# Kernel tuning notes

Hardware: AMD Instinct MI355X
Metric: run time of the kernel (lower is better)

Reference implementation:

```python
import math
import jax, jax.numpy as jnp
import numpy as np

EMBED_DIM = 768
NUM_HEADS = 12
HEAD_DIM = EMBED_DIM // NUM_HEADS


def setup_inputs() -> dict:
    key = jax.random.key(0)
    ks = jax.random.split(key, 9)
    R, C, B, E = 128, 512, 1, EMBED_DIM
    x = jax.random.normal(ks[0], (R, C, B, E), dtype=jnp.float32)
    s = 0.02
    # weights stored so that projection is x @ W + b (i.e. torch Linear weight transposed)
    Wq = jax.random.normal(ks[1], (E, E), dtype=jnp.float32) * s
    Wk = jax.random.normal(ks[2], (E, E), dtype=jnp.float32) * s
    Wv = jax.random.normal(ks[3], (E, E), dtype=jnp.float32) * s
    Wo = jax.random.normal(ks[4], (E, E), dtype=jnp.float32) * s
    bq = jnp.zeros((E,), jnp.float32)
    bk = jnp.zeros((E,), jnp.float32)
    bv = jnp.zeros((E,), jnp.float32)
    bo = jnp.zeros((E,), jnp.float32)
    return {"x": x, "Wq": Wq, "bq": bq, "Wk": Wk, "bk": bk,
            "Wv": Wv, "bv": bv, "Wo": Wo, "bo": bo}


def reference(x, Wq, bq, Wk, bk, Wv, bv, Wo, bo):
    R, C, B, E = x.shape
    H, D = NUM_HEADS, HEAD_DIM
    # scaling = head_dim^-0.5 / sqrt(num_rows)  (align_scaling)
    scaling = (D ** -0.5) / math.sqrt(R)
    q = (x @ Wq + bq).reshape(R, C, B, H, D) * scaling
    k = (x @ Wk + bk).reshape(R, C, B, H, D)
    v = (x @ Wv + bv).reshape(R, C, B, H, D)
    # sum attention logits over rows r -> shared [h, n, i, j] attention map
    attn_weights = jnp.einsum('rinhd,rjnhd->hnij', q, k)
    attn_probs = jax.nn.softmax(attn_weights, axis=-1)
    context = jnp.einsum('hnij,rjnhd->rinhd', attn_probs, v)
    context = context.reshape(R, C, B, E)
    output = context @ Wo + bo
    return output, attn_probs
```

## Files before the change

kernel.cpp:

```cpp
#include <hip/hip_runtime.h>
#include <math.h>

#define RDIM 128
#define CDIM 512
#define EDIM 768
#define HDIM 12
#define DDIM 64
#define MDIM (RDIM*CDIM)
#define OUT_ELEMS ((size_t)MDIM*EDIM)
#define HSTRIDE ((size_t)CDIM*RDIM*DDIM)
#define WELEMS (EDIM*EDIM)

typedef unsigned short ushort_t;
typedef __attribute__((ext_vector_type(8))) short bf16x8;
typedef __attribute__((ext_vector_type(8))) unsigned short u16x8;
typedef __attribute__((ext_vector_type(4))) float f32x4;

__device__ __forceinline__ ushort_t f2bf(float f) {
    unsigned u = __float_as_uint(f);
    unsigned r = u + 0x7fffu + ((u >> 16) & 1u);
    return (ushort_t)(r >> 16);
}

__device__ __forceinline__ void gload16(const void* g, void* l) {
    __builtin_amdgcn_global_load_lds(
        (const __attribute__((address_space(1))) unsigned int*)g,
        (__attribute__((address_space(3))) unsigned int*)l, 16, 0, 0);
}

__global__ __launch_bounds__(256)
void cast_x(const float* __restrict__ x, ushort_t* __restrict__ xb) {
    size_t i = ((size_t)blockIdx.x * 256 + threadIdx.x) * 8;
    float4 a = *(const float4*)&x[i];
    float4 b = *(const float4*)&x[i + 4];
    u16x8 o;
    o[0]=f2bf(a.x); o[1]=f2bf(a.y); o[2]=f2bf(a.z); o[3]=f2bf(a.w);
    o[4]=f2bf(b.x); o[5]=f2bf(b.y); o[6]=f2bf(b.z); o[7]=f2bf(b.w);
    *(u16x8*)&xb[i] = o;
}

__global__ __launch_bounds__(256)
void transpose_cast_w(const float* __restrict__ W, ushort_t* __restrict__ Wt) {
    __shared__ ushort_t t[64][66];
    const int k0 = blockIdx.x * 64, n0 = blockIdx.y * 64;
    const int tx = threadIdx.x & 15, ty = threadIdx.x >> 4;
    #pragma unroll
    for (int rep = 0; rep < 4; ++rep) {
        int k = ty + rep * 16;
        float4 v = *(const float4*)&W[(size_t)(k0 + k) * EDIM + n0 + tx*4];
        t[k][tx*4+0] = f2bf(v.x); t[k][tx*4+1] = f2bf(v.y);
        t[k][tx*4+2] = f2bf(v.z); t[k][tx*4+3] = f2bf(v.w);
    }
    __syncthreads();
    #pragma unroll
    for (int rep = 0; rep < 4; ++rep) {
        int n = ty + rep * 16;
        ushort4 o = { t[tx*4+0][n], t[tx*4+1][n], t[tx*4+2][n], t[tx*4+3][n] };
        *(ushort4*)&Wt[(size_t)(n0 + n) * EDIM + k0 + tx*4] = o;
    }
}

__global__ __launch_bounds__(256)
void concat_bias(const float* __restrict__ bq, const float* __restrict__ bk,
                 const float* __restrict__ bv, float* __restrict__ bqkv) {
    int i = blockIdx.x * 256 + threadIdx.x;
    if (i < 768)        bqkv[i] = bq[i];
    else if (i < 1536)  bqkv[i] = bk[i - 768];
    else if (i < 2304)  bqkv[i] = bv[i - 1536];
}

#define SBAR do { __builtin_amdgcn_sched_barrier(0); \
                  __builtin_amdgcn_s_barrier(); \
                  __builtin_amdgcn_sched_barrier(0); } while(0)
#define SCHED0 __builtin_amdgcn_sched_barrier(0)
#define VMCNT(n_) asm volatile("s_waitcnt vmcnt(" #n_ ")" ::: "memory")

template<int M, int N, int K, int LDK, int MODE, int NWG>
__global__ __launch_bounds__(512, 2)
void gemm8(const ushort_t* __restrict__ A, const ushort_t* __restrict__ B,
           const float* __restrict__ bias, float scale,
           float* __restrict__ outF, ushort_t* __restrict__ outB,
           size_t sAh, size_t sBh) {
    __shared__ __align__(16) char smem[131072];
    constexpr int NT = K / 64;

    const int tid = threadIdx.x;
    const int lane = tid & 63, wid = tid >> 6;
    const int wr = wid >> 2, wc = wid & 3;
    const int fr = lane & 15, fs = lane >> 4;
    const int sw = (fr & 7) << 3;

    const int bid = blockIdx.x;
    const int w = (bid & 7) * (NWG / 8) + (bid >> 3);
    int bm, bn, h = 0, ksub = 0, plane = 0, ntile = 0;
    if (MODE == 4)      { ntile = w % 9; bm = (w / 9) * 256; bn = ntile * 256; }
    else if (MODE == 2) { plane = w >> 2; h = plane >> 3; ksub = plane & 7;
                          bm = ((w >> 1) & 1) * 256; bn = (w & 1) * 256; }
    else if (MODE == 3) { h = w >> 6; bm = ((w >> 5) & 1) * 256; bn = (w & 31) * 256; }
    else                { bm = (w / 3) * 256; bn = (w % 3) * 256; }

    const ushort_t* Ab = A + (MODE == 2 || MODE == 3 ? (size_t)h * sAh : 0)
                       + (MODE == 2 ? (size_t)ksub * K : 0) + (size_t)bm * LDK;
    const ushort_t* Bb = B + (MODE == 2 || MODE == 3 ? (size_t)h * sBh : 0)
                       + (MODE == 2 ? (size_t)ksub * K : 0) + (size_t)bn * LDK;

    const int r0 = tid >> 3, s0 = tid & 7;
    const size_t gO0 = (size_t)r0 * LDK + ((s0 ^ (r0 & 7)) * 8);
    const size_t gO1 = gO0 + (size_t)64 * LDK;
    const int l0 = tid * 16, l1 = tid * 16 + 8192;

#define STAGE_A(t_, h_) do { \
    char* d_ = smem + ((((t_) & 1) * 2 + (h_)) * 16384); \
    const ushort_t* s_ = Ab + (size_t)((h_) * 128) * LDK + (t_) * 64; \
    gload16(s_ + gO0, d_ + l0); gload16(s_ + gO1, d_ + l1); } while(0)
#define STAGE_B(t_, h_) do { \
    char* d_ = smem + 65536 + ((((t_) & 1) * 2 + (h_)) * 16384); \
    const ushort_t* s_ = Bb + (size_t)((h_) * 128) * LDK + (t_) * 64; \
    gload16(s_ + gO0, d_ + l0); gload16(s_ + gO1, d_ + l1); } while(0)

    f32x4 acc[8][4];
    #pragma unroll
    for (int i = 0; i < 8; ++i)
        #pragma unroll
        for (int j = 0; j < 4; ++j) acc[i][j] = (f32x4){0.f, 0.f, 0.f, 0.f};
    bf16x8 a_[4][2], bb0_[2][2], bb1_[2][2];

#define DSA(t_, mq_) do { \
    const ushort_t* As_ = (const ushort_t*)(smem + ((((t_) & 1) * 2 + wr) * 16384)); \
    _Pragma("unroll") for (int f = 0; f < 4; ++f) \
      _Pragma("unroll") for (int kk = 0; kk < 2; ++kk) \
        a_[f][kk] = *(const bf16x8*)&As_[((mq_) * 64 + f * 16 + fr) * 64 \
                                          + ((kk * 32 + fs * 8) ^ sw)]; } while(0)

#define DSB(t_, nq_, B_) do { \
    const ushort_t* Bs_ = (const ushort_t*)(smem + 65536 + ((((t_) & 1) * 2 + (wc >> 1)) * 16384)); \
    _Pragma("unroll") for (int nf = 0; nf < 2; ++nf) \
      _Pragma("unroll") for (int kk = 0; kk < 2; ++kk) \
        B_[nf][kk] = *(const bf16x8*)&Bs_[((wc & 1) * 64 + (nq_) * 32 + nf * 16 + fr) * 64 \
                                           + ((kk * 32 + fs * 8) ^ sw)]; } while(0)

#define MFMA8(mq_, nq_, B_) do { \
    __builtin_amdgcn_s_setprio(1); \
    _Pragma("unroll") for (int f = 0; f < 4; ++f) \
      _Pragma("unroll") for (int nf2 = 0; nf2 < 2; ++nf2) \
        _Pragma("unroll") for (int kk = 0; kk < 2; ++kk) \
          acc[(mq_) * 4 + f][(nq_) * 2 + nf2] = __builtin_amdgcn_mfma_f32_16x16x32_bf16( \
              a_[f][kk], B_[nf2][kk], acc[(mq_) * 4 + f][(nq_) * 2 + nf2], 0, 0, 0); \
    __builtin_amdgcn_s_setprio(0); } while(0)

    STAGE_B(0, 0); SCHED0;
    STAGE_B(0, 1); SCHED0;
    STAGE_A(0, 0); SCHED0;
    STAGE_A(0, 1); SCHED0;
    STAGE_B(1, 0); SCHED0;
    STAGE_B(1, 1); SCHED0;
    STAGE_A(1, 0); SCHED0;
    STAGE_A(1, 1); SCHED0;
    VMCNT(8);
    SBAR;

    for (int t = 0; t < NT - 2; ++t) {
        DSA(t, 0); DSB(t, 0, bb0_);
        MFMA8(0, 0, bb0_);
        SBAR;
        DSB(t, 1, bb1_);
        MFMA8(0, 1, bb1_);
        SBAR;
        DSA(t, 1);
        STAGE_B(t + 2, 0); STAGE_B(t + 2, 1);
        MFMA8(1, 0, bb0_);
        SBAR;
        STAGE_A(t + 2, 0); STAGE_A(t + 2, 1);
        MFMA8(1, 1, bb1_);
        VMCNT(8);
        SBAR;
    }

    {
        const int t = NT - 2;
        DSA(t, 0); DSB(t, 0, bb0_); MFMA8(0, 0, bb0_); SBAR;
        DSB(t, 1, bb1_);            MFMA8(0, 1, bb1_); SBAR;
        DSA(t, 1);                  MFMA8(1, 0, bb0_); SBAR;
        MFMA8(1, 1, bb1_);
        VMCNT(0);
        SBAR;
        const int u = NT - 1;
        DSA(u, 0); DSB(u, 0, bb0_); MFMA8(0, 0, bb0_); SBAR;
        DSB(u, 1, bb1_);            MFMA8(0, 1, bb1_); SBAR;
        DSA(u, 1);                  MFMA8(1, 0, bb0_); SBAR;
        MFMA8(1, 1, bb1_);
    }

    if (MODE == 4) {
        const int which = ntile / 3;
        const int hcb = (ntile % 3) * 256;
        if (which < 2) {
            ushort_t* dst = outB + (size_t)which * OUT_ELEMS;
            const float sc = (which == 0) ? scale : 1.f;
            #pragma unroll
            for (int mf = 0; mf < 8; ++mf) {
                #pragma unroll
                for (int nf = 0; nf < 4; ++nf) {
                    const int hcol = hcb + wc*64 + nf*16 + fr;
                    const float bv = bias[which*768 + hcol];
                    const int hh = hcol >> 6, d = hcol & 63;
                    #pragma unroll
                    for (int j = 0; j < 4; ++j) {
                        const int m = bm + wr*128 + mf*16 + fs*4 + j;
                        float v = (acc[mf][nf][j] + bv) * sc;
                        size_t addr = (size_t)hh * HSTRIDE
                                    + (size_t)(m & 511) * 8192 + (m >> 9) * 64 + d;
                        dst[addr] = f2bf(v);
                    }
                }
            }
        } else {
            ushort_t* Ts = (ushort_t*)smem;
            ushort_t* dst = outB + 2 * OUT_ELEMS;
            const int rblk = bm >> 9, jb = bm & 511;
            __syncthreads();
            #pragma unroll
            for (int q = 0; q < 2; ++q) {
                if ((wc >> 1) == q) {
                    #pragma unroll
                    for (int mf = 0; mf < 8; ++mf) {
                        #pragma unroll
                        for (int nf = 0; nf < 4; ++nf) {
                            const int nl = wc*64 + nf*16 + fr;
                            const float bv = bias[1536 + hcb + nl];
                            #pragma unroll
                            for (int j = 0; j < 4; ++j)
                                Ts[(nl & 127)*264 + wr*128 + mf*16 + fs*4 + j] =
                                    f2bf(acc[mf][nf][j] + bv);
                        }
                    }
                }
                __syncthreads();
                #pragma unroll
                for (int it = 0; it < 8; ++it) {
                    const int idx = it * 512 + tid;
                    const int row = idx >> 5, c8 = (idx & 31) * 8;
                    const int nl = q*128 + row;
                    const int hh = (hcb + nl) >> 6, d = nl & 63;
                    uint4 wv;
                    wv.x = *(const uint*)&Ts[row*264 + c8];
                    wv.y = *(const uint*)&Ts[row*264 + c8 + 2];
                    wv.z = *(const uint*)&Ts[row*264 + c8 + 4];
                    wv.w = *(const uint*)&Ts[row*264 + c8 + 6];
                    size_t addr = (size_t)hh * HSTRIDE
                                + (size_t)(rblk*64 + d) * CDIM + jb + c8;
                    *(uint4*)&dst[addr] = wv;
                }
                __syncthreads();
            }
        }
        return;
    }

    #pragma unroll
    for (int mf = 0; mf < 8; ++mf) {
        #pragma unroll
        for (int nf = 0; nf < 4; ++nf) {
            const int n = bn + wc*64 + nf*16 + fr;
            float bv = (MODE == 1) ? bias[n] : 0.f;
            #pragma unroll
            for (int j = 0; j < 4; ++j) {
                const int m = bm + wr*128 + mf*16 + fs*4 + j;
                float v = acc[mf][nf][j];
                if (MODE == 1) {
                    outF[(size_t)m * N + n] = v + bv;
                } else if (MODE == 2) {
                    outF[(size_t)plane * (CDIM*CDIM) + (size_t)m * CDIM + n] = v;
                } else {
                    size_t addr = ((size_t)(n >> 6) * CDIM + m) * EDIM
                                + h * DDIM + (n & 63);
                    outB[addr] = f2bf(v);
                }
            }
        }
    }
}

__global__ __launch_bounds__(256)
void softmax_reduce(const float* __restrict__ part, float* __restrict__ attn,
                    ushort_t* __restrict__ Pb) {
    const int row = blockIdx.x;
    const int h = row >> 9, c = row & 511;
    const int tid = threadIdx.x;
    const int lane = tid & 63, wid = tid >> 6;
    __shared__ float red[8];

    float v0 = 0.f, v1 = 0.f;
    #pragma unroll
    for (int s = 0; s < 8; ++s) {
        const float* p = part + ((size_t)(h*8 + s) * (CDIM*CDIM)) + (size_t)c * CDIM;
        v0 += p[tid];
        v1 += p[tid + 256];
    }
    float m = fmaxf(v0, v1);
    #pragma unroll
    for (int off = 32; off > 0; off >>= 1) m = fmaxf(m, __shfl_down(m, off));
    if (lane == 0) red[wid] = m;
    __syncthreads();
    if (tid == 0) red[4] = fmaxf(fmaxf(red[0], red[1]), fmaxf(red[2], red[3]));
    __syncthreads();
    const float M = red[4];

    float e0 = expf(v0 - M), e1 = expf(v1 - M);
    float s = e0 + e1;
    #pragma unroll
    for (int off = 32; off > 0; off >>= 1) s += __shfl_down(s, off);
    __syncthreads();
    if (lane == 0) red[wid] = s;
    __syncthreads();
    if (tid == 0) red[5] = red[0] + red[1] + red[2] + red[3];
    __syncthreads();
    const float inv = 1.f / red[5];
    float o0 = e0 * inv, o1 = e1 * inv;
    float* pout = attn + (size_t)row * CDIM;
    ushort_t* pb = Pb + (size_t)row * CDIM;
    pout[tid] = o0;        pout[tid + 256] = o1;
    pb[tid]   = f2bf(o0);  pb[tid + 256]   = f2bf(o1);
}

extern "C" void kernel_launch(void* const* d_in, const int* in_sizes, int n_in,
                              void* d_out, int out_size, void* d_ws, size_t ws_size,
                              hipStream_t stream) {
    const float* x  = (const float*)d_in[0];
    const float* Wq = (const float*)d_in[1];
    const float* bq = (const float*)d_in[2];
    const float* Wk = (const float*)d_in[3];
    const float* bk = (const float*)d_in[4];
    const float* Wv = (const float*)d_in[5];
    const float* bv = (const float*)d_in[6];
    const float* Wo = (const float*)d_in[7];
    const float* bo = (const float*)d_in[8];

    float* out   = (float*)d_out;
    float* attnp = out + OUT_ELEMS;

    ushort_t* ws   = (ushort_t*)d_ws;
    ushort_t* xb   = ws;
    ushort_t* Wqkv = xb + OUT_ELEMS;
    ushort_t* Wto  = Wqkv + 3*WELEMS;
    float*    bqkv = (float*)(Wto + WELEMS);
    ushort_t* Qp   = Wto + WELEMS + 4608;
    ushort_t* Kp   = Qp + OUT_ELEMS;
    ushort_t* Vt   = Kp + OUT_ELEMS;
    ushort_t* Pb   = Vt + OUT_ELEMS;
    float*    part = (float*)xb;
    ushort_t* ctxb = xb;

    const float scaling = 0.011048543456039806f;

    cast_x<<<MDIM*EDIM/(256*8), 256, 0, stream>>>(x, xb);
    dim3 wt(EDIM/64, EDIM/64);
    transpose_cast_w<<<wt, 256, 0, stream>>>(Wq, Wqkv);
    transpose_cast_w<<<wt, 256, 0, stream>>>(Wk, Wqkv + WELEMS);
    transpose_cast_w<<<wt, 256, 0, stream>>>(Wv, Wqkv + 2*WELEMS);
    transpose_cast_w<<<wt, 256, 0, stream>>>(Wo, Wto);
    concat_bias<<<9, 256, 0, stream>>>(bq, bk, bv, bqkv);

    gemm8<MDIM, 2304, EDIM, EDIM, 4, 2304><<<2304, 512, 0, stream>>>(
        xb, Wqkv, bqkv, scaling, nullptr, Qp, 0, 0);

    gemm8<CDIM, CDIM, 1024, 8192, 2, 384><<<384, 512, 0, stream>>>(
        Qp, Kp, nullptr, 1.f, part, nullptr, HSTRIDE, HSTRIDE);

    softmax_reduce<<<HDIM*CDIM, 256, 0, stream>>>(part, attnp, Pb);

    gemm8<CDIM, 8192, CDIM, CDIM, 3, 768><<<768, 512, 0, stream>>>(
        Pb, Vt, nullptr, 1.f, nullptr, ctxb, (size_t)CDIM*CDIM, HSTRIDE);

    gemm8<MDIM, EDIM, EDIM, EDIM, 1, 768><<<768, 512, 0, stream>>>(
        ctxb, Wto, bo, 1.f, out, nullptr, 0, 0);
}
```

Baseline: 581.8 us.

## Software-pipeline LDS fragment loads one stage ahead of MFMA in GEMM main loop

Adds a second A-fragment register set and reorders the main loop so each LDS read (the B fragments for the next quarter, the A fragments for the next half, and the first A/B fragments of the next k-tile) is issued one MFMA block ahead of its use. The aim is to hide LDS read latency behind MFMA work instead of stalling right before each MFMA group. The global-load wait moves earlier and becomes a full vmcnt(0), and register pressure rises from the extra fragment buffers, which may lower occupancy.

```diff
diff --git a/kernel.cpp b/kernel.cpp
--- a/kernel.cpp
+++ b/kernel.cpp
@@ -123,13 +123,13 @@
     for (int i = 0; i < 8; ++i)
         #pragma unroll
         for (int j = 0; j < 4; ++j) acc[i][j] = (f32x4){0.f, 0.f, 0.f, 0.f};
-    bf16x8 a_[4][2], bb0_[2][2], bb1_[2][2];
-
-#define DSA(t_, mq_) do { \
+    bf16x8 a_[4][2], a2_[4][2], bb0_[2][2], bb1_[2][2];
+
+#define DSA(t_, mq_, A_) do { \
     const ushort_t* As_ = (const ushort_t*)(smem + ((((t_) & 1) * 2 + wr) * 16384)); \
     _Pragma("unroll") for (int f = 0; f < 4; ++f) \
       _Pragma("unroll") for (int kk = 0; kk < 2; ++kk) \
-        a_[f][kk] = *(const bf16x8*)&As_[((mq_) * 64 + f * 16 + fr) * 64 \
+        A_[f][kk] = *(const bf16x8*)&As_[((mq_) * 64 + f * 16 + fr) * 64 \
                                           + ((kk * 32 + fs * 8) ^ sw)]; } while(0)
 
 #define DSB(t_, nq_, B_) do { \
@@ -139,13 +139,13 @@
         B_[nf][kk] = *(const bf16x8*)&Bs_[((wc & 1) * 64 + (nq_) * 32 + nf * 16 + fr) * 64 \
                                            + ((kk * 32 + fs * 8) ^ sw)]; } while(0)
 
-#define MFMA8(mq_, nq_, B_) do { \
+#define MFMA8(mq_, nq_, A_, B_) do { \
     __builtin_amdgcn_s_setprio(1); \
     _Pragma("unroll") for (int f = 0; f < 4; ++f) \
       _Pragma("unroll") for (int nf2 = 0; nf2 < 2; ++nf2) \
         _Pragma("unroll") for (int kk = 0; kk < 2; ++kk) \
           acc[(mq_) * 4 + f][(nq_) * 2 + nf2] = __builtin_amdgcn_mfma_f32_16x16x32_bf16( \
-              a_[f][kk], B_[nf2][kk], acc[(mq_) * 4 + f][(nq_) * 2 + nf2], 0, 0, 0); \
+              A_[f][kk], B_[nf2][kk], acc[(mq_) * 4 + f][(nq_) * 2 + nf2], 0, 0, 0); \
     __builtin_amdgcn_s_setprio(0); } while(0)
 
     STAGE_B(0, 0); SCHED0;
@@ -158,37 +158,38 @@
     STAGE_A(1, 1); SCHED0;
     VMCNT(8);
     SBAR;
+    DSA(0, 0, a_); DSB(0, 0, bb0_);
 
     for (int t = 0; t < NT - 2; ++t) {
-        DSA(t, 0); DSB(t, 0, bb0_);
-        MFMA8(0, 0, bb0_);
+        DSB(t, 1, bb1_);
+        MFMA8(0, 0, a_, bb0_);
         SBAR;
-        DSB(t, 1, bb1_);
-        MFMA8(0, 1, bb1_);
+        DSA(t, 1, a2_);
+        MFMA8(0, 1, a_, bb1_);
+        VMCNT(0);
         SBAR;
-        DSA(t, 1);
+        DSA(t + 1, 0, a_);
         STAGE_B(t + 2, 0); STAGE_B(t + 2, 1);
-        MFMA8(1, 0, bb0_);
+        MFMA8(1, 0, a2_, bb0_);
         SBAR;
+        DSB(t + 1, 0, bb0_);
         STAGE_A(t + 2, 0); STAGE_A(t + 2, 1);
-        MFMA8(1, 1, bb1_);
-        VMCNT(8);
+        MFMA8(1, 1, a2_, bb1_);
         SBAR;
     }
 
     {
         const int t = NT - 2;
-        DSA(t, 0); DSB(t, 0, bb0_); MFMA8(0, 0, bb0_); SBAR;
-        DSB(t, 1, bb1_);            MFMA8(0, 1, bb1_); SBAR;
-        DSA(t, 1);                  MFMA8(1, 0, bb0_); SBAR;
-        MFMA8(1, 1, bb1_);
-        VMCNT(0);
-        SBAR;
+        DSB(t, 1, bb1_);      MFMA8(0, 0, a_, bb0_);  SBAR;
+        DSA(t, 1, a2_);       MFMA8(0, 1, a_, bb1_);
+        VMCNT(0);             SBAR;
+        DSA(t + 1, 0, a_);    MFMA8(1, 0, a2_, bb0_); SBAR;
+        DSB(t + 1, 0, bb0_);  MFMA8(1, 1, a2_, bb1_); SBAR;
         const int u = NT - 1;
-        DSA(u, 0); DSB(u, 0, bb0_); MFMA8(0, 0, bb0_); SBAR;
-        DSB(u, 1, bb1_);            MFMA8(0, 1, bb1_); SBAR;
-        DSA(u, 1);                  MFMA8(1, 0, bb0_); SBAR;
-        MFMA8(1, 1, bb1_);
+        DSB(u, 1, bb1_);      MFMA8(0, 0, a_, bb0_);  SBAR;
+        DSA(u, 1, a2_);       MFMA8(0, 1, a_, bb1_);  SBAR;
+        MFMA8(1, 0, a2_, bb0_);
+        MFMA8(1, 1, a2_, bb1_);
     }
 
     if (MODE == 4) {
```

New measurement: 598.0 us. 1.03x slower.

## Switch GEMMs to 256x128 tiles with B fragments loaded directly from global

Applied to the files above, without the earlier changes.

Replaces the 512-thread 256x256-tile GEMM with a 256-thread 256x128-tile variant. Only A is staged through LDS, with a two-buffer schedule. B fragments now go straight from global memory into registers, double-buffered across k-steps, which removes the B LDS traffic and cuts shared memory use. The risk is uncoalesced, unswizzled global reads for B that can stall the MFMA pipeline. The V-transpose epilogue is also simplified to a single pass.

```diff
diff --git a/kernel.cpp b/kernel.cpp
--- a/kernel.cpp
+++ b/kernel.cpp
@@ -76,54 +76,55 @@
 #define VMCNT(n_) asm volatile("s_waitcnt vmcnt(" #n_ ")" ::: "memory")
 
 template<int M, int N, int K, int LDK, int MODE, int NWG>
-__global__ __launch_bounds__(512, 2)
-void gemm8(const ushort_t* __restrict__ A, const ushort_t* __restrict__ B,
+__global__ __launch_bounds__(256, 2)
+void gemm2(const ushort_t* __restrict__ A, const ushort_t* __restrict__ B,
            const float* __restrict__ bias, float scale,
            float* __restrict__ outF, ushort_t* __restrict__ outB,
            size_t sAh, size_t sBh) {
-    __shared__ __align__(16) char smem[131072];
+    __shared__ __align__(16) char smem[69632];
     constexpr int NT = K / 64;
 
     const int tid = threadIdx.x;
     const int lane = tid & 63, wid = tid >> 6;
-    const int wr = wid >> 2, wc = wid & 3;
+    const int wr = wid >> 1, wc = wid & 1;
     const int fr = lane & 15, fs = lane >> 4;
     const int sw = (fr & 7) << 3;
 
     const int bid = blockIdx.x;
     const int w = (bid & 7) * (NWG / 8) + (bid >> 3);
     int bm, bn, h = 0, ksub = 0, plane = 0, ntile = 0;
-    if (MODE == 4)      { ntile = w % 9; bm = (w / 9) * 256; bn = ntile * 256; }
-    else if (MODE == 2) { plane = w >> 2; h = plane >> 3; ksub = plane & 7;
-                          bm = ((w >> 1) & 1) * 256; bn = (w & 1) * 256; }
-    else if (MODE == 3) { h = w >> 6; bm = ((w >> 5) & 1) * 256; bn = (w & 31) * 256; }
-    else                { bm = (w / 3) * 256; bn = (w % 3) * 256; }
+    if (MODE == 4)      { ntile = w % 18; bm = (w / 18) * 256; bn = ntile * 128; }
+    else if (MODE == 2) { plane = w >> 3; h = plane >> 3; ksub = plane & 7;
+                          bm = ((w >> 2) & 1) * 256; bn = (w & 3) * 128; }
+    else if (MODE == 3) { h = w >> 7; bm = ((w >> 6) & 1) * 256; bn = (w & 63) * 128; }
+    else                { bm = (w / 6) * 256; bn = (w % 6) * 128; }
 
     const ushort_t* Ab = A + (MODE == 2 || MODE == 3 ? (size_t)h * sAh : 0)
                        + (MODE == 2 ? (size_t)ksub * K : 0) + (size_t)bm * LDK;
     const ushort_t* Bb = B + (MODE == 2 || MODE == 3 ? (size_t)h * sBh : 0)
                        + (MODE == 2 ? (size_t)ksub * K : 0) + (size_t)bn * LDK;
 
-    const int r0 = tid >> 3, s0 = tid & 7;
-    const size_t gO0 = (size_t)r0 * LDK + ((s0 ^ (r0 & 7)) * 8);
-    const size_t gO1 = gO0 + (size_t)64 * LDK;
-    const int l0 = tid * 16, l1 = tid * 16 + 8192;
+    size_t gOf[4]; int lOf[4];
+    #pragma unroll
+    for (int j = 0; j < 4; ++j) {
+        int ci = j * 256 + tid;
+        int row = ci >> 3, seg = ci & 7;
+        gOf[j] = (size_t)row * LDK + (size_t)(((seg ^ (row & 7)) * 8));
+        lOf[j] = ci * 16;
+    }
 
 #define STAGE_A(t_, h_) do { \
     char* d_ = smem + ((((t_) & 1) * 2 + (h_)) * 16384); \
     const ushort_t* s_ = Ab + (size_t)((h_) * 128) * LDK + (t_) * 64; \
-    gload16(s_ + gO0, d_ + l0); gload16(s_ + gO1, d_ + l1); } while(0)
-#define STAGE_B(t_, h_) do { \
-    char* d_ = smem + 65536 + ((((t_) & 1) * 2 + (h_)) * 16384); \
-    const ushort_t* s_ = Bb + (size_t)((h_) * 128) * LDK + (t_) * 64; \
-    gload16(s_ + gO0, d_ + l0); gload16(s_ + gO1, d_ + l1); } while(0)
+    gload16(s_ + gOf[0], d_ + lOf[0]); gload16(s_ + gOf[1], d_ + lOf[1]); \
+    gload16(s_ + gOf[2], d_ + lOf[2]); gload16(s_ + gOf[3], d_ + lOf[3]); } while(0)
 
     f32x4 acc[8][4];
     #pragma unroll
     for (int i = 0; i < 8; ++i)
         #pragma unroll
         for (int j = 0; j < 4; ++j) acc[i][j] = (f32x4){0.f, 0.f, 0.f, 0.f};
-    bf16x8 a_[4][2], bb0_[2][2], bb1_[2][2];
+    bf16x8 a_[4][2], bb0x[2][2], bb1x[2][2], bb0y[2][2], bb1y[2][2];
 
 #define DSA(t_, mq_) do { \
     const ushort_t* As_ = (const ushort_t*)(smem + ((((t_) & 1) * 2 + wr) * 16384)); \
@@ -132,12 +133,11 @@
         a_[f][kk] = *(const bf16x8*)&As_[((mq_) * 64 + f * 16 + fr) * 64 \
                                           + ((kk * 32 + fs * 8) ^ sw)]; } while(0)
 
-#define DSB(t_, nq_, B_) do { \
-    const ushort_t* Bs_ = (const ushort_t*)(smem + 65536 + ((((t_) & 1) * 2 + (wc >> 1)) * 16384)); \
+#define BLOAD(t_, nq_, B_) do { \
     _Pragma("unroll") for (int nf = 0; nf < 2; ++nf) \
       _Pragma("unroll") for (int kk = 0; kk < 2; ++kk) \
-        B_[nf][kk] = *(const bf16x8*)&Bs_[((wc & 1) * 64 + (nq_) * 32 + nf * 16 + fr) * 64 \
-                                           + ((kk * 32 + fs * 8) ^ sw)]; } while(0)
+        B_[nf][kk] = *(const bf16x8*)(Bb + (size_t)(wc*64 + (nq_)*32 + nf*16 + fr) * LDK \
+                                         + (t_)*64 + kk*32 + fs*8); } while(0)
 
 #define MFMA8(mq_, nq_, B_) do { \
     __builtin_amdgcn_s_setprio(1); \
@@ -148,52 +148,37 @@
               a_[f][kk], B_[nf2][kk], acc[(mq_) * 4 + f][(nq_) * 2 + nf2], 0, 0, 0); \
     __builtin_amdgcn_s_setprio(0); } while(0)
 
-    STAGE_B(0, 0); SCHED0;
-    STAGE_B(0, 1); SCHED0;
-    STAGE_A(0, 0); SCHED0;
-    STAGE_A(0, 1); SCHED0;
-    STAGE_B(1, 0); SCHED0;
-    STAGE_B(1, 1); SCHED0;
-    STAGE_A(1, 0); SCHED0;
-    STAGE_A(1, 1); SCHED0;
+#define TILE(t_, C0_, C1_, N0_, N1_, STG_, BLD_, VM_) do { \
+    DSA(t_, 0); \
+    if (STG_) { STAGE_A((t_) + 1, 0); STAGE_A((t_) + 1, 1); } \
+    MFMA8(0, 0, C0_); \
+    MFMA8(0, 1, C1_); \
+    SBAR; \
+    DSA(t_, 1); \
+    if (BLD_) { BLOAD((t_) + 1, 0, N0_); BLOAD((t_) + 1, 1, N1_); } \
+    MFMA8(1, 0, C0_); \
+    MFMA8(1, 1, C1_); \
+    SCHED0; \
+    if (VM_) VMCNT(8); \
+    SBAR; } while(0)
+
+    STAGE_A(0, 0); STAGE_A(0, 1);
+    SCHED0;
+    BLOAD(0, 0, bb0x); BLOAD(0, 1, bb1x);
+    SCHED0;
     VMCNT(8);
     SBAR;
 
-    for (int t = 0; t < NT - 2; ++t) {
-        DSA(t, 0); DSB(t, 0, bb0_);
-        MFMA8(0, 0, bb0_);
-        SBAR;
-        DSB(t, 1, bb1_);
-        MFMA8(0, 1, bb1_);
-        SBAR;
-        DSA(t, 1);
-        STAGE_B(t + 2, 0); STAGE_B(t + 2, 1);
-        MFMA8(1, 0, bb0_);
-        SBAR;
-        STAGE_A(t + 2, 0); STAGE_A(t + 2, 1);
-        MFMA8(1, 1, bb1_);
-        VMCNT(8);
-        SBAR;
-    }
-
-    {
-        const int t = NT - 2;
-        DSA(t, 0); DSB(t, 0, bb0_); MFMA8(0, 0, bb0_); SBAR;
-        DSB(t, 1, bb1_);            MFMA8(0, 1, bb1_); SBAR;
-        DSA(t, 1);                  MFMA8(1, 0, bb0_); SBAR;
-        MFMA8(1, 1, bb1_);
-        VMCNT(0);
-        SBAR;
-        const int u = NT - 1;
-        DSA(u, 0); DSB(u, 0, bb0_); MFMA8(0, 0, bb0_); SBAR;
-        DSB(u, 1, bb1_);            MFMA8(0, 1, bb1_); SBAR;
-        DSA(u, 1);                  MFMA8(1, 0, bb0_); SBAR;
-        MFMA8(1, 1, bb1_);
-    }
+    for (int t = 0; t < NT - 2; t += 2) {
+        TILE(t,     bb0x, bb1x, bb0y, bb1y, 1, 1, 1);
+        TILE(t + 1, bb0y, bb1y, bb0x, bb1x, 1, 1, 1);
+    }
+    TILE(NT - 2, bb0x, bb1x, bb0y, bb1y, 1, 1, 1);
+    TILE(NT - 1, bb0y, bb1y, bb0x, bb1x, 0, 0, 0);
 
     if (MODE == 4) {
-        const int which = ntile / 3;
-        const int hcb = (ntile % 3) * 256;
+        const int which = ntile / 6;
+        const int nb = (ntile % 6) * 128;
         if (which < 2) {
             ushort_t* dst = outB + (size_t)which * OUT_ELEMS;
             const float sc = (which == 0) ? scale : 1.f;
@@ -201,7 +186,7 @@
             for (int mf = 0; mf < 8; ++mf) {
                 #pragma unroll
                 for (int nf = 0; nf < 4; ++nf) {
-                    const int hcol = hcb + wc*64 + nf*16 + fr;
+                    const int hcol = nb + wc*64 + nf*16 + fr;
                     const float bv = bias[which*768 + hcol];
                     const int hh = hcol >> 6, d = hcol & 63;
                     #pragma unroll
@@ -220,38 +205,31 @@
             const int rblk = bm >> 9, jb = bm & 511;
             __syncthreads();
             #pragma unroll
-            for (int q = 0; q < 2; ++q) {
-                if ((wc >> 1) == q) {
+            for (int mf = 0; mf < 8; ++mf) {
+                #pragma unroll
+                for (int nf = 0; nf < 4; ++nf) {
+                    const int nl = wc*64 + nf*16 + fr;
+                    const float bv = bias[1536 + nb + nl];
                     #pragma unroll
-                    for (int mf = 0; mf < 8; ++mf) {
-                        #pragma unroll
-                        for (int nf = 0; nf < 4; ++nf) {
-                            const int nl = wc*64 + nf*16 + fr;
-                            const float bv = bias[1536 + hcb + nl];
-                            #pragma unroll
-                            for (int j = 0; j < 4; ++j)
-                                Ts[(nl & 127)*264 + wr*128 + mf*16 + fs*4 + j] =
-                                    f2bf(acc[mf][nf][j] + bv);
-                        }
-                    }
+                    for (int j = 0; j < 4; ++j)
+                        Ts[nl*264 + wr*128 + mf*16 + fs*4 + j] =
+                            f2bf(acc[mf][nf][j] + bv);
                 }
-                __syncthreads();
-                #pragma unroll
-                for (int it = 0; it < 8; ++it) {
-                    const int idx = it * 512 + tid;
-                    const int row = idx >> 5, c8 = (idx & 31) * 8;
-                    const int nl = q*128 + row;
-                    const int hh = (hcb + nl) >> 6, d = nl & 63;
-                    uint4 wv;
-                    wv.x = *(const uint*)&Ts[row*264 + c8];
-                    wv.y = *(const uint*)&Ts[row*264 + c8 + 2];
-                    wv.z = *(const uint*)&Ts[row*264 + c8 + 4];
-                    wv.w = *(const uint*)&Ts[row*264 + c8 + 6];
-                    size_t addr = (size_t)hh * HSTRIDE
-                                + (size_t)(rblk*64 + d) * CDIM + jb + c8;
-                    *(uint4*)&dst[addr] = wv;
-                }
-                __syncthreads();
+            }
+            __syncthreads();
+            #pragma unroll
+            for (int it = 0; it < 16; ++it) {
+                const int idx = it * 256 + tid;
+                const int row = idx >> 5, c8 = (idx & 31) * 8;
+                const int hh = (nb + row) >> 6, d = (nb + row) & 63;
+                uint4 wv;
+                wv.x = *(const uint*)&Ts[row*264 + c8];
+                wv.y = *(const uint*)&Ts[row*264 + c8 + 2];
+                wv.z = *(const uint*)&Ts[row*264 + c8 + 4];
+                wv.w = *(const uint*)&Ts[row*264 + c8 + 6];
+                size_t addr = (size_t)hh * HSTRIDE
+                            + (size_t)(rblk*64 + d) * CDIM + jb + c8;
+                *(uint4*)&dst[addr] = wv;
             }
         }
         return;
@@ -361,17 +339,17 @@
     transpose_cast_w<<<wt, 256, 0, stream>>>(Wo, Wto);
     concat_bias<<<9, 256, 0, stream>>>(bq, bk, bv, bqkv);
 
-    gemm8<MDIM, 2304, EDIM, EDIM, 4, 2304><<<2304, 512, 0, stream>>>(
+    gemm2<MDIM, 2304, EDIM, EDIM, 4, 4608><<<4608, 256, 0, stream>>>(
         xb, Wqkv, bqkv, scaling, nullptr, Qp, 0, 0);
 
-    gemm8<CDIM, CDIM, 1024, 8192, 2, 384><<<384, 512, 0, stream>>>(
+    gemm2<CDIM, CDIM, 1024, 8192, 2, 768><<<768, 256, 0, stream>>>(
         Qp, Kp, nullptr, 1.f, part, nullptr, HSTRIDE, HSTRIDE);
 
     softmax_reduce<<<HDIM*CDIM, 256, 0, stream>>>(part, attnp, Pb);
 
-    gemm8<CDIM, 8192, CDIM, CDIM, 3, 768><<<768, 512, 0, stream>>>(
+    gemm2<CDIM, 8192, CDIM, CDIM, 3, 1536><<<1536, 256, 0, stream>>>(
         Pb, Vt, nullptr, 1.f, nullptr, ctxb, (size_t)CDIM*CDIM, HSTRIDE);
 
-    gemm8<MDIM, EDIM, EDIM, EDIM, 1, 768><<<768, 512, 0, stream>>>(
+    gemm2<MDIM, EDIM, EDIM, EDIM, 1, 1536><<<1536, 256, 0, stream>>>(
         ctxb, Wto, bo, 1.f, out, nullptr, 0, 0);
 }
```

After: 860.7 us. 47.9% more time.
